# Performance work log

Hardware: AMD Instinct MI355X
Metric: run time of the kernel (lower is better)

Reference implementation:

```python
import jax, jax.numpy as jnp
import numpy as np

MAX_FREQ = 4
OMEGA = 0.5 * np.pi
PATCH = 64


def _unnorm(c, size):
    # align_corners=False convention of torch.grid_sample
    return ((c + 1.0) * size - 1.0) / 2.0


def _gather(im, yy, xx):
    # im [C,H,W], yy/xx [Ho,Wo] -> [C,Ho,Wo]
    return im[:, yy, xx]


def _gs_nearest(inp, grid):
    # inp [B,C,H,W], grid [B,Ho,Wo,2] (x,y); padding_mode='border'
    B, C, H, W = inp.shape
    x = jnp.clip(jnp.round(_unnorm(grid[..., 0], W)), 0, W - 1).astype(jnp.int32)
    y = jnp.clip(jnp.round(_unnorm(grid[..., 1], H)), 0, H - 1).astype(jnp.int32)
    return jax.vmap(_gather)(inp, y, x)  # [B,C,Ho,Wo]


def _gs_bilinear(inp, grid):
    B, C, H, W = inp.shape
    x = jnp.clip(_unnorm(grid[..., 0], W), 0.0, W - 1.0)
    y = jnp.clip(_unnorm(grid[..., 1], H), 0.0, H - 1.0)
    x0 = jnp.floor(x); y0 = jnp.floor(y)
    wx = (x - x0)[:, None]; wy = (y - y0)[:, None]  # [B,1,Ho,Wo]
    x0i = x0.astype(jnp.int32); y0i = y0.astype(jnp.int32)
    x1i = jnp.minimum(x0i + 1, W - 1); y1i = jnp.minimum(y0i + 1, H - 1)
    g = jax.vmap(_gather)
    v00 = g(inp, y0i, x0i); v01 = g(inp, y0i, x1i)
    v10 = g(inp, y1i, x0i); v11 = g(inp, y1i, x1i)
    return (v00 * (1 - wx) * (1 - wy) + v01 * wx * (1 - wy)
            + v10 * (1 - wx) * wy + v11 * wx * wy)


def _conv2d(x, w, b):
    y = jax.lax.conv_general_dilated(x, w, (1, 1), ((1, 1), (1, 1)),
                                     dimension_numbers=("NCHW", "OIHW", "NCHW"))
    return y + b[None, :, None, None]


def _lc_decoder(q, rel):
    # q [B,Ho,Wo,2F+1], rel [B,Ho,Wo,1]; Fourier basis [1, cos(k*w*rel), sin(k*w*rel)]
    k = jnp.arange(1, MAX_FREQ + 1, dtype=q.dtype)
    ang = rel * k * OMEGA  # [B,Ho,Wo,F]
    basis = jnp.concatenate([jnp.ones_like(rel), jnp.cos(ang), jnp.sin(ang)], axis=-1)
    return jnp.sum(q * basis, axis=-1, keepdims=True)  # [B,Ho,Wo,1]


def _forward(sinogram, feat, grid, square_inv, adapt_w, adapt_b):
    B = feat.shape[0]
    sino = _conv2d(feat, adapt_w, adapt_b)          # [B,2F+1,V,D]
    V, D = sino.shape[-2], sino.shape[-1]
    # make_coord along detector axis (dim=1 coord channel), padding=0
    coord_d = ((jnp.arange(D, dtype=sino.dtype) + 0.5) / D) * 2.0 - 1.0
    sino_coord = jnp.broadcast_to(coord_d[None, None, None, :], (B, 1, V, D))
    shift_interval = 1.0 / D
    eps = 1e-4
    q_recons, lengths = [], []
    for sx in (-shift_interval, shift_interval):  # ensembling shifts
        g = grid + jnp.array([sx, 0.0], dtype=grid.dtype) + 1e-6
        q_recon = jnp.transpose(_gs_nearest(sino, g), (0, 2, 3, 1))       # [B,V,P2,2F+1]
        q_coord = jnp.transpose(_gs_nearest(sino_coord, g), (0, 2, 3, 1))  # [B,V,P2,1]
        rel = (grid[..., 0:1] - q_coord) * D
        q_recons.append(_lc_decoder(q_recon, rel))
        lengths.append(jnp.abs(rel) + eps)
    tot = lengths[0] + lengths[1]
    # lengths are swapped before weighting (cross weighting)
    recon = q_recons[0] * lengths[1] / tot + q_recons[1] * lengths[0] / tot
    out = jnp.sum(jnp.transpose(recon, (0, 3, 1, 2)) * square_inv * 10000.0, axis=-2)
    # back projection of center channel of raw sinogram
    ch = sinogram.shape[1]
    bp = _gs_bilinear(sinogram[:, ch // 2:ch // 2 + 1], grid)
    out = out + jnp.sum(bp * square_inv * 10000.0, axis=-2)  # [B,1,P2]
    return out.reshape(B, 1, PATCH, PATCH)


def setup_inputs() -> dict:
    key = jax.random.key(0)
    ks = jax.random.split(key, 6)
    B, V, D, ENC = 4, 360, 512, 64
    P2 = PATCH * PATCH
    CH = 2 * MAX_FREQ + 1
    return {
        "sinogram": jax.random.normal(ks[0], (B, 1, V, D), jnp.float32),
        "feat": jax.random.normal(ks[1], (B, ENC, V, D), jnp.float32),
        "grid": jax.random.uniform(ks[2], (B, V, P2, 2), jnp.float32, -1.0, 1.0),
        "square_inv": jax.random.uniform(ks[3], (B, 1, V, P2), jnp.float32, 1e-5, 1e-4),
        "adapt_w": jax.random.normal(ks[4], (CH, ENC, 3, 3), jnp.float32) * 0.05,
        "adapt_b": jax.random.normal(ks[5], (CH,), jnp.float32) * 0.05,
    }


def reference(sinogram, feat, grid, square_inv, adapt_w, adapt_b):
    return _forward(sinogram, feat, grid, square_inv, adapt_w, adapt_b)
```

## Files before the change

kernel.cpp:

```cpp
#include <hip/hip_runtime.h>
#include <hip/hip_fp16.h>
#include <math.h>

#define B   4
#define V   360
#define D   512
#define ENC 64
#define CH  9
#define P2  4096
#define NCHUNK 90
#define VCHUNK 4
#define RECH 16
#define PENT 513
#define PENTB 64

template <int PAIR>
__global__ __launch_bounds__(256) void conv_kernel(
    const float* __restrict__ feat,
    const float* __restrict__ w,
    const float* __restrict__ bias,
    char* __restrict__ outp)
{
    const int bid = blockIdx.x;
    const int sw  = (bid & 7) * 180 + (bid >> 3);
    const int b   = sw / V;
    const int v   = sw % V;
    const int d0  = threadIdx.x * 2;

    float acc[CH][2];
    #pragma unroll
    for (int oc = 0; oc < CH; ++oc) {
        const float bv = bias[oc];
        acc[oc][0] = bv; acc[oc][1] = bv;
    }

    const float* fb = feat + ((size_t)b * ENC * V + v) * D + d0;
    const bool vm = v > 0, vp = v < V - 1;
    const bool dm = d0 > 0, dp = d0 + 2 < D;

    float r0[3][4], r1[3][4];

    auto ld = [&](float r[3][4], int ic) {
        const float* f = fb + (size_t)ic * (V * D);
        #pragma unroll
        for (int rr = 0; rr < 3; ++rr) {
            const float* fr = f + (rr - 1) * D;
            const bool ok = (rr == 0) ? vm : ((rr == 2) ? vp : true);
            float2 c = ok ? *(const float2*)fr : float2{0.f, 0.f};
            r[rr][1] = c.x; r[rr][2] = c.y;
            r[rr][0] = (ok && dm) ? fr[-1] : 0.f;
            r[rr][3] = (ok && dp) ? fr[2]  : 0.f;
        }
    };
    auto fmab = [&](const float r[3][4], int ic) {
        #pragma unroll
        for (int oc = 0; oc < CH; ++oc) {
            const float* ww = w + ((size_t)oc * ENC + ic) * 9;
            #pragma unroll
            for (int kr = 0; kr < 3; ++kr) {
                #pragma unroll
                for (int kc = 0; kc < 3; ++kc) {
                    const float wv = ww[kr * 3 + kc];
                    acc[oc][0] = fmaf(r[kr][kc],     wv, acc[oc][0]);
                    acc[oc][1] = fmaf(r[kr][kc + 1], wv, acc[oc][1]);
                }
            }
        }
    };

    ld(r0, 0);
    #pragma unroll 1
    for (int ic = 0; ic < ENC; ic += 2) {
        ld(r1, ic + 1);
        fmab(r0, ic);
        if (ic + 2 < ENC) ld(r0, ic + 2);
        fmab(r1, ic + 1);
    }

    #pragma unroll
    for (int p = 0; p < 2; ++p) {
        union { __half2 h; unsigned u; } cv;
        uint4 pk;
        cv.h = __floats2half2_rn(acc[0][p], acc[1][p]); pk.x = cv.u;
        cv.h = __floats2half2_rn(acc[2][p], acc[3][p]); pk.y = cv.u;
        cv.h = __floats2half2_rn(acc[4][p], acc[5][p]); pk.z = cv.u;
        cv.h = __floats2half2_rn(acc[6][p], acc[7][p]); pk.w = cv.u;
        cv.h = __floats2half2_rn(acc[8][p], 0.f);
        const unsigned short z = (unsigned short)(cv.u & 0xffffu);
        const int x = d0 + p;
        if (PAIR) {
            char* row = outp + (size_t)(b * V + v) * PENT * PENTB;
            char* eA = row + (size_t)(x + 1) * PENTB;
            *(uint4*)eA = pk;
            *(unsigned short*)(eA + 32) = z;
            char* eB = row + (size_t)x * PENTB + 16;
            *(uint4*)eB = pk;
            *(unsigned short*)(eB + 18) = z;
            if (x == 0) {
                *(uint4*)row = pk;
                *(unsigned short*)(row + 32) = z;
            }
            if (x == D - 1) {
                char* eC = row + (size_t)512 * PENTB + 16;
                *(uint4*)eC = pk;
                *(unsigned short*)(eC + 18) = z;
            }
        } else {
            __half* rec = (__half*)outp + (size_t)(((size_t)b * V + v) * D + x) * RECH;
            *(uint4*)rec = pk;
            *(unsigned*)(rec + 8) = (unsigned)z;
        }
    }
}

__global__ __launch_bounds__(256) void build_sg2(
    const float* __restrict__ sg, float2* __restrict__ sg2)
{
    const int i = blockIdx.x * 256 + threadIdx.x;
    const int x = i & (D - 1);
    const float a = sg[i];
    const float c = (x == D - 1) ? a : sg[i + 1];
    sg2[i] = float2{a, c};
}

__device__ __forceinline__ float decode_rec(uint4 a, unsigned short z, float rel)
{
    float q[9];
    union { unsigned uu; __half2 h; } c;
    float2 f;
    c.uu = a.x; f = __half22float2(c.h); q[0] = f.x; q[1] = f.y;
    c.uu = a.y; f = __half22float2(c.h); q[2] = f.x; q[3] = f.y;
    c.uu = a.z; f = __half22float2(c.h); q[4] = f.x; q[5] = f.y;
    c.uu = a.w; f = __half22float2(c.h); q[6] = f.x; q[7] = f.y;
    union { unsigned short us; __half hh; } c2;
    c2.us = z;
    q[8] = __half2float(c2.hh);

    const float ang = rel * 1.5707963267948966f;
    float s1, c1;
    __sincosf(ang, &s1, &c1);
    const float c2f = fmaf(2.f * c1, c1, -1.f);
    const float s2f = 2.f * c1 * s1;
    const float c3f = fmaf(2.f * c1, c2f, -c1);
    const float s3f = fmaf(2.f * c1, s2f, -s1);
    const float c4f = fmaf(2.f * c1, c3f, -c2f);
    const float s4f = fmaf(2.f * c1, s3f, -s2f);

    float vv = q[0];
    vv = fmaf(q[1], c1,  vv); vv = fmaf(q[2], c2f, vv);
    vv = fmaf(q[3], c3f, vv); vv = fmaf(q[4], c4f, vv);
    vv = fmaf(q[5], s1,  vv); vv = fmaf(q[6], s2f, vv);
    vv = fmaf(q[7], s3f, vv); vv = fmaf(q[8], s4f, vv);
    return vv;
}

__global__ __launch_bounds__(256) void sample_pair(
    const char* __restrict__ pair,
    const float2* __restrict__ sg2,
    const float* __restrict__ grid,
    const float* __restrict__ sq,
    float* __restrict__ partial)
{
    const int bid = blockIdx.x;
    const int xcd = bid & 7;
    const int b   = xcd >> 1;
    const int idx = ((bid >> 3) << 1) | (xcd & 1);
    const int chunk = idx >> 4;
    const int p  = (idx & 15) * 256 + threadIdx.x;
    const int v0 = chunk * VCHUNK;

    const char*   pb  = pair + (size_t)b * V * PENT * PENTB;
    const float2* s2b = sg2 + (size_t)b * V * D;

    float gx[4], gy[4], sv[4];
    #pragma unroll
    for (int u = 0; u < 4; ++u) {
        const size_t gi = (size_t)(b * V + v0 + u) * P2 + p;
        const double gd = __builtin_nontemporal_load((const double*)grid + gi);
        const unsigned long long gu = __double_as_longlong(gd);
        gx[u] = __uint_as_float((unsigned)gu);
        gy[u] = __uint_as_float((unsigned)(gu >> 32));
        sv[u] = __builtin_nontemporal_load(sq + gi);
    }

    uint4 qa[4], qb[4];
    unsigned short zA[4], zB[4];
    float relm[4], relp[4];
    #pragma unroll
    for (int u = 0; u < 4; ++u) {
        const float fy = ((gy[u] + 1e-6f + 1.f) * (float)V - 1.f) * 0.5f;
        const int   yi = (int)fminf(fmaxf(rintf(fy), 0.f), (float)(V - 1));
        const float fx0 = ((gx[u] + 1e-6f + 1.f) * (float)D - 1.f) * 0.5f;
        const int xm = (int)fminf(fmaxf(rintf(fx0 - 0.5f), 0.f), (float)(D - 1));
        const int xp = (int)fminf(fmaxf(rintf(fx0 + 0.5f), 0.f), (float)(D - 1));
        const float qcm = ((float)xm + 0.5f) * (2.f / (float)D) - 1.f;
        const float qcp = ((float)xp + 0.5f) * (2.f / (float)D) - 1.f;
        relm[u] = (gx[u] - qcm) * (float)D;
        relp[u] = (gx[u] - qcp) * (float)D;
        const char* rowp = pb + (size_t)yi * (PENT * PENTB);
        const char* e1 = rowp + (size_t)(xm + 1) * PENTB;
        const char* e2 = rowp + (size_t)xp * PENTB;
        qa[u] = *(const uint4*)e1;
        zA[u] = *(const unsigned short*)(e1 + 32);
        qb[u] = *(const uint4*)(e2 + 16);
        zB[u] = *(const unsigned short*)(e2 + 34);
    }

    float bl00[4], bl01[4], bl10[4], bl11[4], wxv[4], wyv[4];
    #pragma unroll
    for (int u = 0; u < 4; ++u) {
        float fxb = fminf(fmaxf(((gx[u] + 1.f) * (float)D - 1.f) * 0.5f, 0.f), (float)(D - 1));
        float fyb = fminf(fmaxf(((gy[u] + 1.f) * (float)V - 1.f) * 0.5f, 0.f), (float)(V - 1));
        const float x0 = floorf(fxb), y0 = floorf(fyb);
        wxv[u] = fxb - x0; wyv[u] = fyb - y0;
        const int x0i = (int)x0, y0i = (int)y0;
        const int y1i = min(y0i + 1, V - 1);
        const float2 t  = s2b[y0i * D + x0i];
        const float2 u2 = s2b[y1i * D + x0i];
        bl00[u] = t.x;  bl01[u] = t.y;
        bl10[u] = u2.x; bl11[u] = u2.y;
    }

    float acc = 0.f;
    #pragma unroll
    for (int u = 0; u < 4; ++u) {
        const float vmv = decode_rec(qa[u], zA[u], relm[u]);
        const float vpv = decode_rec(qb[u], zB[u], relp[u]);
        const float lm = fabsf(relm[u]) + 1e-4f;
        const float lp = fabsf(relp[u]) + 1e-4f;
        const float recon = (vmv * lp + vpv * lm) / (lm + lp);

        const float wx = wxv[u], wy = wyv[u];
        const float bp = bl00[u] * (1.f - wx) * (1.f - wy) + bl01[u] * wx * (1.f - wy)
                       + bl10[u] * (1.f - wx) * wy         + bl11[u] * wx * wy;

        acc += (recon + bp) * sv[u] * 1e4f;
    }
    __builtin_nontemporal_store(acc, partial + ((size_t)chunk * B + b) * P2 + p);
}

template <int PAIRED>
__global__ __launch_bounds__(256) void sample_basic(
    const __half* __restrict__ sino,
    const float* __restrict__ sinogram,
    const float2* __restrict__ sg2,
    const float* __restrict__ grid,
    const float* __restrict__ sq,
    float* __restrict__ partial)
{
    const int bid = blockIdx.x;
    const int xcd = bid & 7;
    const int b   = xcd >> 1;
    const int idx = ((bid >> 3) << 1) | (xcd & 1);
    const int chunk = idx >> 4;
    const int p  = (idx & 15) * 256 + threadIdx.x;
    const int v0 = chunk * VCHUNK;

    const float*  sg   = sinogram + (size_t)b * V * D;
    const float2* s2b  = sg2 + (size_t)b * V * D;
    const __half* sb   = sino + (size_t)b * V * D * RECH;

    float gx[4], gy[4], sv[4];
    #pragma unroll
    for (int u = 0; u < 4; ++u) {
        const size_t gi = (size_t)(b * V + v0 + u) * P2 + p;
        const double gd = __builtin_nontemporal_load((const double*)grid + gi);
        const unsigned long long gu = __double_as_longlong(gd);
        gx[u] = __uint_as_float((unsigned)gu);
        gy[u] = __uint_as_float((unsigned)(gu >> 32));
        sv[u] = __builtin_nontemporal_load(sq + gi);
    }

    uint4    ra[4][2];
    unsigned rz[4][2];
    float    rel[4][2];
    #pragma unroll
    for (int u = 0; u < 4; ++u) {
        const float fy = ((gy[u] + 1e-6f + 1.f) * (float)V - 1.f) * 0.5f;
        const int   yi = (int)fminf(fmaxf(rintf(fy), 0.f), (float)(V - 1));
        const float fx0 = ((gx[u] + 1e-6f + 1.f) * (float)D - 1.f) * 0.5f;
        #pragma unroll
        for (int sft = 0; sft < 2; ++sft) {
            const float fx = (sft == 0) ? (fx0 - 0.5f) : (fx0 + 0.5f);
            const int   xi = (int)fminf(fmaxf(rintf(fx), 0.f), (float)(D - 1));
            const float qc = ((float)xi + 0.5f) * (2.f / (float)D) - 1.f;
            rel[u][sft] = (gx[u] - qc) * (float)D;
            const __half* rec = sb + (size_t)(yi * D + xi) * RECH;
            ra[u][sft] = *(const uint4*)rec;
            rz[u][sft] = *(const unsigned*)(rec + 8);
        }
    }

    float bl00[4], bl01[4], bl10[4], bl11[4], wxv[4], wyv[4];
    #pragma unroll
    for (int u = 0; u < 4; ++u) {
        float fxb = fminf(fmaxf(((gx[u] + 1.f) * (float)D - 1.f) * 0.5f, 0.f), (float)(D - 1));
        float fyb = fminf(fmaxf(((gy[u] + 1.f) * (float)V - 1.f) * 0.5f, 0.f), (float)(V - 1));
        const float x0 = floorf(fxb), y0 = floorf(fyb);
        wxv[u] = fxb - x0; wyv[u] = fyb - y0;
        const int x0i = (int)x0, y0i = (int)y0;
        const int y1i = min(y0i + 1, V - 1);
        if (PAIRED) {
            const float2 t  = s2b[y0i * D + x0i];
            const float2 u2 = s2b[y1i * D + x0i];
            bl00[u] = t.x;  bl01[u] = t.y;
            bl10[u] = u2.x; bl11[u] = u2.y;
        } else {
            const int x1i = min(x0i + 1, D - 1);
            bl00[u] = sg[y0i * D + x0i]; bl01[u] = sg[y0i * D + x1i];
            bl10[u] = sg[y1i * D + x0i]; bl11[u] = sg[y1i * D + x1i];
        }
    }

    float acc = 0.f;
    #pragma unroll
    for (int u = 0; u < 4; ++u) {
        const float v0f = decode_rec(ra[u][0], (unsigned short)(rz[u][0] & 0xffffu), rel[u][0]);
        const float v1f = decode_rec(ra[u][1], (unsigned short)(rz[u][1] & 0xffffu), rel[u][1]);
        const float l0 = fabsf(rel[u][0]) + 1e-4f;
        const float l1 = fabsf(rel[u][1]) + 1e-4f;
        const float recon = (v0f * l1 + v1f * l0) / (l0 + l1);
        const float wx = wxv[u], wy = wyv[u];
        const float bp = bl00[u] * (1.f - wx) * (1.f - wy) + bl01[u] * wx * (1.f - wy)
                       + bl10[u] * (1.f - wx) * wy         + bl11[u] * wx * wy;
        acc += (recon + bp) * sv[u] * 1e4f;
    }
    __builtin_nontemporal_store(acc, partial + ((size_t)chunk * B + b) * P2 + p);
}

__global__ __launch_bounds__(256) void reduce_kernel(
    const float* __restrict__ partial, float* __restrict__ out)
{
    const int i = blockIdx.x * 256 + threadIdx.x;
    float a = 0.f;
    #pragma unroll 6
    for (int c = 0; c < NCHUNK; ++c)
        a += __builtin_nontemporal_load(partial + (size_t)c * B * P2 + i);
    out[i] = a;
}

extern "C" void kernel_launch(void* const* d_in, const int* in_sizes, int n_in,
                              void* d_out, int out_size, void* d_ws, size_t ws_size,
                              hipStream_t stream)
{
    const float* sinogram = (const float*)d_in[0];
    const float* feat     = (const float*)d_in[1];
    const float* grid     = (const float*)d_in[2];
    const float* sq       = (const float*)d_in[3];
    const float* w        = (const float*)d_in[4];
    const float* bias     = (const float*)d_in[5];
    float* out = (float*)d_out;

    const size_t pair_b = (size_t)B * V * PENT * PENTB;
    const size_t part_b = (size_t)NCHUNK * B * P2 * sizeof(float);
    const size_t sg2_b  = (size_t)B * V * D * sizeof(float2);
    const size_t rec_b  = (size_t)B * V * D * RECH * sizeof(__half);

    if (ws_size >= pair_b + part_b + sg2_b) {
        char*   pair    = (char*)d_ws;
        float*  partial = (float*)((char*)d_ws + pair_b);
        float2* sg2     = (float2*)((char*)d_ws + pair_b + part_b);
        conv_kernel<1><<<dim3(1440), 256, 0, stream>>>(feat, w, bias, pair);
        build_sg2<<<dim3(2880), 256, 0, stream>>>(sinogram, sg2);
        sample_pair<<<dim3(5760), 256, 0, stream>>>(pair, sg2, grid, sq, partial);
        reduce_kernel<<<dim3((B * P2) / 256), 256, 0, stream>>>(partial, out);
    } else if (ws_size >= rec_b + part_b + sg2_b) {
        char*   sino    = (char*)d_ws;
        float*  partial = (float*)((char*)d_ws + rec_b);
        float2* sg2     = (float2*)((char*)d_ws + rec_b + part_b);
        conv_kernel<0><<<dim3(1440), 256, 0, stream>>>(feat, w, bias, sino);
        build_sg2<<<dim3(2880), 256, 0, stream>>>(sinogram, sg2);
        sample_basic<1><<<dim3(5760), 256, 0, stream>>>((const __half*)sino, sinogram, sg2, grid, sq, partial);
        reduce_kernel<<<dim3((B * P2) / 256), 256, 0, stream>>>(partial, out);
    } else {
        char*   sino    = (char*)d_ws;
        float*  partial = (float*)((char*)d_ws + rec_b);
        conv_kernel<0><<<dim3(1440), 256, 0, stream>>>(feat, w, bias, sino);
        sample_basic<0><<<dim3(5760), 256, 0, stream>>>((const __half*)sino, sinogram, (const float2*)sino, grid, sq, partial);
        reduce_kernel<<<dim3((B * P2) / 256), 256, 0, stream>>>(partial, out);
    }
}
```

Before: 315.0 us.

## Stage conv weights in LDS, compute four outputs per thread and two rows per block

The conv kernel now copies all weights into shared memory in a padded, transposed [ic][oc][12] layout so they can be read as float4. Each thread now computes four detector columns instead of two, and each block covers two view rows, so the grid size is halved. Wider per-thread tiles reuse each loaded feature value across more outputs and cut per-block overhead, at the cost of more registers (36 accumulators plus two 18-value input buffers) and a shared-memory prologue in every block. Scheduling barriers are also added in the sampling kernels to separate the gather loads from the arithmetic.

```diff
diff --git a/kernel.cpp b/kernel.cpp
--- a/kernel.cpp
+++ b/kernel.cpp
@@ -21,48 +21,66 @@
     const float* __restrict__ bias,
     char* __restrict__ outp)
 {
+    __shared__ float wl[ENC * CH * 12];
+    for (int i = threadIdx.x; i < ENC * CH * 9; i += 256) {
+        const int oc  = i / (ENC * 9);
+        const int rem = i - oc * (ENC * 9);
+        const int ic  = rem / 9;
+        const int k   = rem - ic * 9;
+        wl[(ic * CH + oc) * 12 + k] = w[i];
+    }
+    __syncthreads();
+
     const int bid = blockIdx.x;
-    const int sw  = (bid & 7) * 180 + (bid >> 3);
-    const int b   = sw / V;
-    const int v   = sw % V;
-    const int d0  = threadIdx.x * 2;
-
-    float acc[CH][2];
+    const int sw  = (bid & 7) * 90 + (bid >> 3);
+    const int b   = sw / 180;
+    const int vt  = sw % 180;
+    const int tr  = threadIdx.x >> 7;
+    const int v   = vt * 2 + tr;
+    const int d0  = (threadIdx.x & 127) * 4;
+
+    float acc[CH][4];
     #pragma unroll
     for (int oc = 0; oc < CH; ++oc) {
         const float bv = bias[oc];
-        acc[oc][0] = bv; acc[oc][1] = bv;
+        #pragma unroll
+        for (int p = 0; p < 4; ++p) acc[oc][p] = bv;
     }
 
     const float* fb = feat + ((size_t)b * ENC * V + v) * D + d0;
     const bool vm = v > 0, vp = v < V - 1;
-    const bool dm = d0 > 0, dp = d0 + 2 < D;
-
-    float r0[3][4], r1[3][4];
-
-    auto ld = [&](float r[3][4], int ic) {
+    const bool dm = d0 > 0, dp = d0 + 4 < D;
+
+    float r0[3][6], r1[3][6];
+
+    auto ld = [&](float r[3][6], int ic) {
         const float* f = fb + (size_t)ic * (V * D);
         #pragma unroll
         for (int rr = 0; rr < 3; ++rr) {
             const float* fr = f + (rr - 1) * D;
             const bool ok = (rr == 0) ? vm : ((rr == 2) ? vp : true);
-            float2 c = ok ? *(const float2*)fr : float2{0.f, 0.f};
-            r[rr][1] = c.x; r[rr][2] = c.y;
+            float4 c = ok ? *(const float4*)fr : float4{0.f, 0.f, 0.f, 0.f};
+            r[rr][1] = c.x; r[rr][2] = c.y; r[rr][3] = c.z; r[rr][4] = c.w;
             r[rr][0] = (ok && dm) ? fr[-1] : 0.f;
-            r[rr][3] = (ok && dp) ? fr[2]  : 0.f;
+            r[rr][5] = (ok && dp) ? fr[4]  : 0.f;
         }
     };
-    auto fmab = [&](const float r[3][4], int ic) {
+    auto fmab = [&](const float r[3][6], int ic) {
         #pragma unroll
         for (int oc = 0; oc < CH; ++oc) {
-            const float* ww = w + ((size_t)oc * ENC + ic) * 9;
+            const float* wp = &wl[(ic * CH + oc) * 12];
+            const float4 wA = *(const float4*)wp;
+            const float4 wB = *(const float4*)(wp + 4);
+            const float  w8 = wp[8];
+            const float wk[9] = {wA.x, wA.y, wA.z, wA.w, wB.x, wB.y, wB.z, wB.w, w8};
             #pragma unroll
             for (int kr = 0; kr < 3; ++kr) {
                 #pragma unroll
                 for (int kc = 0; kc < 3; ++kc) {
-                    const float wv = ww[kr * 3 + kc];
-                    acc[oc][0] = fmaf(r[kr][kc],     wv, acc[oc][0]);
-                    acc[oc][1] = fmaf(r[kr][kc + 1], wv, acc[oc][1]);
+                    const float wv = wk[kr * 3 + kc];
+                    #pragma unroll
+                    for (int p = 0; p < 4; ++p)
+                        acc[oc][p] = fmaf(r[kr][p + kc], wv, acc[oc][p]);
                 }
             }
         }
@@ -78,7 +96,7 @@
     }
 
     #pragma unroll
-    for (int p = 0; p < 2; ++p) {
+    for (int p = 0; p < 4; ++p) {
         union { __half2 h; unsigned u; } cv;
         uint4 pk;
         cv.h = __floats2half2_rn(acc[0][p], acc[1][p]); pk.x = cv.u;
@@ -221,6 +239,8 @@
         bl10[u] = u2.x; bl11[u] = u2.y;
     }
 
+    __builtin_amdgcn_sched_barrier(0);
+
     float acc = 0.f;
     #pragma unroll
     for (int u = 0; u < 4; ++u) {
@@ -312,6 +332,8 @@
         }
     }
 
+    __builtin_amdgcn_sched_barrier(0);
+
     float acc = 0.f;
     #pragma unroll
     for (int u = 0; u < 4; ++u) {
@@ -360,7 +382,7 @@
         char*   pair    = (char*)d_ws;
         float*  partial = (float*)((char*)d_ws + pair_b);
         float2* sg2     = (float2*)((char*)d_ws + pair_b + part_b);
-        conv_kernel<1><<<dim3(1440), 256, 0, stream>>>(feat, w, bias, pair);
+        conv_kernel<1><<<dim3(720), 256, 0, stream>>>(feat, w, bias, pair);
         build_sg2<<<dim3(2880), 256, 0, stream>>>(sinogram, sg2);
         sample_pair<<<dim3(5760), 256, 0, stream>>>(pair, sg2, grid, sq, partial);
         reduce_kernel<<<dim3((B * P2) / 256), 256, 0, stream>>>(partial, out);
@@ -368,14 +390,14 @@
         char*   sino    = (char*)d_ws;
         float*  partial = (float*)((char*)d_ws + rec_b);
         float2* sg2     = (float2*)((char*)d_ws + rec_b + part_b);
-        conv_kernel<0><<<dim3(1440), 256, 0, stream>>>(feat, w, bias, sino);
+        conv_kernel<0><<<dim3(720), 256, 0, stream>>>(feat, w, bias, sino);
         build_sg2<<<dim3(2880), 256, 0, stream>>>(sinogram, sg2);
         sample_basic<1><<<dim3(5760), 256, 0, stream>>>((const __half*)sino, sinogram, sg2, grid, sq, partial);
         reduce_kernel<<<dim3((B * P2) / 256), 256, 0, stream>>>(partial, out);
     } else {
         char*   sino    = (char*)d_ws;
         float*  partial = (float*)((char*)d_ws + rec_b);
-        conv_kernel<0><<<dim3(1440), 256, 0, stream>>>(feat, w, bias, sino);
+        conv_kernel<0><<<dim3(720), 256, 0, stream>>>(feat, w, bias, sino);
         sample_basic<0><<<dim3(5760), 256, 0, stream>>>((const __half*)sino, sinogram, (const float2*)sino, grid, sq, partial);
         reduce_kernel<<<dim3((B * P2) / 256), 256, 0, stream>>>(partial, out);
     }
```

New measurement: 341.9 us. +8.5%, slower.
